# Optimization experiments

Measured on AMD Instinct MI355X. Metric: run time of the kernel, lower is better.

The kernel has to match this reference:

```python
import jax, jax.numpy as jnp
import numpy as np
from math import pi as PI

K = 32
CUTOFF = 10.0
F = 128          # num_filters (also num_gaussians)
H = 256          # in_channels
N_CLASSES = 7
N_IND = 8
LOG2 = float(np.log(2.0))


def _ssp(x):
    # ShiftedSoftplus
    return jax.nn.softplus(x) - LOG2


def _gaussian_smearing(d):
    # d: [E, 1] -> [E, F]; torch_geometric GaussianSmearing(start=0, stop=cutoff)
    offset = jnp.linspace(0.0, CUTOFF, F, dtype=d.dtype)            # [F]
    coeff = -0.5 / (offset[1] - offset[0]) ** 2
    return jnp.exp(coeff * (d - offset[None, :]) ** 2)


def setup_inputs() -> dict:
    key = jax.random.key(0)
    ks = jax.random.split(key, 24)
    Nq, Nc, B = 8192, 16384, 8
    box = 20.0
    pos_query = jax.random.uniform(ks[0], (Nq, 3), dtype=jnp.float32) * box
    pos_ctx = jax.random.uniform(ks[1], (Nc, 3), dtype=jnp.float32) * box
    node_attr_ctx = jax.random.normal(ks[2], (Nc, H), dtype=jnp.float32)
    batch_query = jnp.sort(jax.random.randint(ks[3], (Nq,), 0, B)).astype(jnp.int32)
    batch_ctx = jnp.sort(jax.random.randint(ks[4], (Nc,), 0, B)).astype(jnp.int32)

    def lin_w(k, fin, fout):
        return (jax.random.normal(k, (fin, fout), dtype=jnp.float32) / np.sqrt(fin)).astype(jnp.float32)

    return {
        "pos_query": pos_query,
        "pos_ctx": pos_ctx,
        "node_attr_ctx": node_attr_ctx,
        "batch_query": batch_query,
        "batch_ctx": batch_ctx,
        "lin1_w": lin_w(ks[5], H, F),                 # bias=False
        "lin2_w": lin_w(ks[6], F, F),
        "lin2_b": jnp.zeros((F,), jnp.float32),
        "nn1_w": lin_w(ks[7], F, F),
        "nn1_b": jnp.zeros((F,), jnp.float32),
        "nn2_w": lin_w(ks[8], F, F),
        "nn2_b": jnp.zeros((F,), jnp.float32),
        "cls1_w": lin_w(ks[9], F, F),
        "cls1_b": jnp.zeros((F,), jnp.float32),
        "cls2_w": lin_w(ks[10], F, N_CLASSES),
        "cls2_b": jnp.zeros((N_CLASSES,), jnp.float32),
        "prop1_w": lin_w(ks[11], F, F),
        "prop1_b": jnp.zeros((F,), jnp.float32),
        "prop2_w": lin_w(ks[12], F, N_IND),
        "prop2_b": jnp.zeros((N_IND,), jnp.float32),
    }


def reference(pos_query, pos_ctx, node_attr_ctx, batch_query, batch_ctx,
              lin1_w, lin2_w, lin2_b, nn1_w, nn1_b, nn2_w, nn2_b,
              cls1_w, cls1_b, cls2_w, cls2_b, prop1_w, prop1_b, prop2_w, prop2_b):
    Nq = pos_query.shape[0]

    # --- batch-aware kNN: for each query, k nearest context points in same graph ---
    d2 = (jnp.sum(pos_query ** 2, -1)[:, None]
          + jnp.sum(pos_ctx ** 2, -1)[None, :]
          - 2.0 * (pos_query @ pos_ctx.T))                            # [Nq, Nc]
    same = batch_query[:, None] == batch_ctx[None, :]
    d2 = jnp.where(same, d2, jnp.inf)
    _, nbr = jax.lax.top_k(-d2, K)                                    # [Nq, K] ctx indices

    # --- gather neighbor data; each query owns exactly K contiguous edges ---
    diff = pos_query[:, None, :] - pos_ctx[nbr]                       # [Nq, K, 3]
    dist = jnp.sqrt(jnp.sum(diff ** 2, -1)).reshape(-1, 1)            # [E, 1]
    attr_j = node_attr_ctx[nbr].reshape(Nq * K, -1)                   # [E, H]

    # --- per-edge filter network on distance expansion ---
    W = _ssp(_gaussian_smearing(dist) @ nn1_w + nn1_b) @ nn2_w + nn2_b  # [E, F]

    h = (W * (attr_j @ lin1_w)) @ lin2_w + lin2_b                     # [E, F]

    # --- cosine cutoff envelope ---
    C = 0.5 * (jnp.cos(dist * (PI / CUTOFF)) + 1.0)
    C = C * (dist <= CUTOFF) * (dist >= 0.0)
    h = h * C                                                         # [E, F]

    # scatter_add by query index == sum over the K contiguous edges per query
    y = jnp.sum(h.reshape(Nq, K, F), axis=1)                          # [Nq, F]

    y_cls = _ssp(y @ cls1_w + cls1_b) @ cls2_w + cls2_b               # [Nq, 7]
    y_ind = _ssp(y @ prop1_w + prop1_b) @ prop2_w + prop2_b           # [Nq, 8]
    return (y_cls, y_ind)
```

## Files before the change

### kernel.cpp

```cpp
#include <hip/hip_runtime.h>
#include <math.h>

#define K 32
#define F 128
#define H 256
#define TAB 4096
#define QB 8
#define BMAX 16
#define RCUT2 100.0f
#define KBINS 64
#define BINCAP 2560
#define BCAP 128
#define FP 132
#define FRR 16

__device__ __forceinline__ float ssp(float x) {
    return fmaxf(x, 0.0f) + log1pf(expf(-fabsf(x))) - 0.69314718055994531f;
}

__device__ __forceinline__ float d2f4(float4 p, float qx, float qy, float qz) {
    float dx = qx - p.x;
    float dy = qy - p.y;
    float dz = qz - p.z;
    return fmaf(dz, dz, fmaf(dy, dy, dx * dx));
}

__global__ __launch_bounds__(256) void prep_kernel(const int* __restrict__ bc, int Nc,
                                                   int* __restrict__ ctx_start,
                                                   const float* __restrict__ posc,
                                                   float4* __restrict__ posc4) {
    int blk = blockIdx.x;
    int tid = threadIdx.x;
    if (blk == 0) {
        if (tid <= BMAX) {
            int b = tid;
            int lo = 0, hi = Nc;
            while (lo < hi) {
                int mid = (lo + hi) >> 1;
                if (bc[mid] < b) lo = mid + 1; else hi = mid;
            }
            ctx_start[b] = lo;
        }
    } else {
        int i = (blk - 1) * 256 + tid;
        if (i < Nc)
            posc4[i] = make_float4(posc[i * 3 + 0], posc[i * 3 + 1], posc[i * 3 + 2], 0.0f);
    }
}


__device__ __forceinline__ void feat_body(char* smem, const float* __restrict__ attr,
                                          const float* __restrict__ lin1_w,
                                          float* __restrict__ ctx_feat, int Nc,
                                          int blk, int tid) {
    float (*sa)[H] = (float (*)[H])smem;
    int r0 = blk * FRR;
    int f = tid & 63;
    int g = tid >> 6;

    {
        float4* dst = (float4*)sa;
        const int total = FRR * H / 4;
        if (r0 + FRR <= Nc) {
            const float4* src = (const float4*)(attr + (size_t)r0 * H);
            for (int i = tid; i < total; i += 256) dst[i] = src[i];
        } else {
            for (int i = tid; i < total; i += 256) {
                int r = i / (H / 4);
                if (r0 + r < Nc) dst[i] = ((const float4*)(attr + (size_t)r0 * H))[i];
                else dst[i] = make_float4(0.0f, 0.0f, 0.0f, 0.0f);
            }
        }
    }
    __syncthreads();

    float acc0[4], acc1[4];
#pragma unroll
    for (int r = 0; r < 4; ++r) { acc0[r] = 0.0f; acc1[r] = 0.0f; }
    for (int k = 0; k < H; k += 4) {
        float wa0 = lin1_w[(k + 0) * F + f];
        float wa1 = lin1_w[(k + 1) * F + f];
        float wa2 = lin1_w[(k + 2) * F + f];
        float wa3 = lin1_w[(k + 3) * F + f];
        float wb0 = lin1_w[(k + 0) * F + f + 64];
        float wb1 = lin1_w[(k + 1) * F + f + 64];
        float wb2 = lin1_w[(k + 2) * F + f + 64];
        float wb3 = lin1_w[(k + 3) * F + f + 64];
#pragma unroll
        for (int r = 0; r < 4; ++r) {
            float4 a4 = *(const float4*)&sa[g * 4 + r][k];
            acc0[r] = fmaf(a4.x, wa0, acc0[r]);
            acc0[r] = fmaf(a4.y, wa1, acc0[r]);
            acc0[r] = fmaf(a4.z, wa2, acc0[r]);
            acc0[r] = fmaf(a4.w, wa3, acc0[r]);
            acc1[r] = fmaf(a4.x, wb0, acc1[r]);
            acc1[r] = fmaf(a4.y, wb1, acc1[r]);
            acc1[r] = fmaf(a4.z, wb2, acc1[r]);
            acc1[r] = fmaf(a4.w, wb3, acc1[r]);
        }
    }
#pragma unroll
    for (int r = 0; r < 4; ++r) {
        int row = r0 + g * 4 + r;
        if (row < Nc) {
            ctx_feat[(size_t)row * F + f] = acc0[r];
            ctx_feat[(size_t)row * F + f + 64] = acc1[r];
        }
    }
}

__device__ __forceinline__ void knn_body(char* smem, const float* __restrict__ posq,
                                         const float4* __restrict__ posc4,
                                         const int* __restrict__ bq,
                                         const int* __restrict__ ctx_start,
                                         int* __restrict__ nbr, int Nq,
                                         int blk, int tid) {
    unsigned char (*sbin)[BINCAP] = (unsigned char (*)[BINCAP])(smem);
    int (*hist)[KBINS]            = (int (*)[KBINS])(smem + 10240);
    unsigned (*bkey)[BCAP]        = (unsigned (*)[BCAP])(smem + 11264);
    int (*bidx)[BCAP]             = (int (*)[BCAP])(smem + 13312);
    int* s_nwin                   = (int*)(smem + 15360);
    int* s_nbnd                   = (int*)(smem + 15376);

    int lane = tid & 63;
    int w = tid >> 6;
    int q = blk * 4 + w;
    bool active = q < Nq;
    int qc = active ? q : 0;

    hist[w][lane] = 0;
    if (lane == 0) { s_nwin[w] = 0; s_nbnd[w] = 0; }

    float qx = posq[qc * 3 + 0];
    float qy = posq[qc * 3 + 1];
    float qz = posq[qc * 3 + 2];
    int b = bq[qc];
    int c0 = ctx_start[b];
    int c1 = ctx_start[b + 1];
    int seg = active ? (c1 - c0) : 0;
    __syncthreads();

    const float SCALE = (float)KBINS / RCUT2;
    int farc = -1;

    for (int i = lane; i < seg; i += 64) {
        float d2 = d2f4(posc4[c0 + i], qx, qy, qz);
        int bin = 255;
        if (d2 < RCUT2) {
            bin = (int)(d2 * SCALE);
            atomicAdd(&hist[w][bin], 1);
        }
        if (i < BINCAP) sbin[w][i] = (unsigned char)bin;
    }
    __syncthreads();

    int h = hist[w][lane];
    int inc = h;
#pragma unroll
    for (int off = 1; off < 64; off <<= 1) {
        int v = __shfl_up(inc, off);
        if (lane >= off) inc += v;
    }
    unsigned long long bal = __ballot(inc >= K);
    int T, below;
    if (bal) {
        T = __ffsll(bal) - 1;
        below = __shfl(inc, T) - __shfl(h, T);
    } else {
        T = KBINS;
        below = __shfl(inc, 63);
    }

    for (int i = lane; i < seg; i += 64) {
        int c = c0 + i;
        int bin;
        if (i < BINCAP) bin = sbin[w][i];
        else {
            float d2 = d2f4(posc4[c], qx, qy, qz);
            bin = (d2 < RCUT2) ? (int)(d2 * SCALE) : 255;
        }
        if (bin < T) {
            int p = atomicAdd(&s_nwin[w], 1);
            nbr[(size_t)q * K + p] = c;
        } else if (bin == T) {
            int p = atomicAdd(&s_nbnd[w], 1);
            if (p < BCAP) {
                float d2 = d2f4(posc4[c], qx, qy, qz);
                bkey[w][p] = __float_as_uint(d2);
                bidx[w][p] = c;
            }
        } else if (bin == 255) {
            farc = c;
        }
    }
#pragma unroll
    for (int off = 1; off < 64; off <<= 1) farc = max(farc, __shfl_xor(farc, off));
    if (farc < 0) farc = c0;
    __syncthreads();

    if (!active) return;
    int nb = min(s_nbnd[w], BCAP);
    int m = K - s_nwin[w];
    for (int it = 0; it < m; ++it) {
        unsigned long long bestkey = 0xFFFFFFFFFFFFFFFFull;
        int bestp = -1;
        for (int p = lane; p < nb; p += 64) {
            unsigned kk = bkey[w][p];
            if (kk != 0xFFFFFFFFu) {
                unsigned long long pk = ((unsigned long long)kk << 32) | (unsigned)bidx[w][p];
                if (pk < bestkey) { bestkey = pk; bestp = p; }
            }
        }
#pragma unroll
        for (int off = 1; off < 64; off <<= 1) {
            unsigned long long ok = __shfl_xor(bestkey, off);
            int op = __shfl_xor(bestp, off);
            if (ok < bestkey) { bestkey = ok; bestp = op; }
        }
        if (lane == 0) {
            if (bestp >= 0 && bestkey != 0xFFFFFFFFFFFFFFFFull) {
                nbr[(size_t)q * K + below + it] = (int)(bestkey & 0xFFFFFFFFu);
                bkey[w][bestp] = 0xFFFFFFFFu;
            } else {
                nbr[(size_t)q * K + below + it] = farc;
            }
        }
        __asm__ volatile("" ::: "memory");
    }
}

__device__ __forceinline__ void wtab_body(char* smem, const float* __restrict__ nn1_w,
                                          const float* __restrict__ nn1_b,
                                          const float* __restrict__ nn2_w,
                                          const float* __restrict__ nn2_b,
                                          float2* __restrict__ wt2,
                                          int blk, int tid) {
    float (*sg)[F] = (float (*)[F])smem;
    float (*st)[F] = (float (*)[F])(smem + 8704);
    int t0 = blk * FRR;
    int f = tid & (F - 1);
    int g = tid >> 7;

    const float delta = 10.0f / 127.0f;
    const float coeff = -0.5f / (delta * delta);
    float off = (float)f * delta;
    for (int r = g; r < 17; r += 2) {
        float dist = (float)(t0 + r) * (10.0f / (float)TAB);
        float d = dist - off;
        sg[r][f] = expf(coeff * d * d);
    }
    __syncthreads();

    float acc[9];
#pragma unroll
    for (int r = 0; r < 9; ++r) acc[r] = 0.0f;
    for (int j = 0; j < F; j += 4) {
        float w0 = nn1_w[(j + 0) * F + f];
        float w1 = nn1_w[(j + 1) * F + f];
        float w2 = nn1_w[(j + 2) * F + f];
        float w3 = nn1_w[(j + 3) * F + f];
#pragma unroll
        for (int r = 0; r < 9; ++r) {
            float4 a4 = *(const float4*)&sg[g * 8 + r][j];
            acc[r] = fmaf(a4.x, w0, acc[r]);
            acc[r] = fmaf(a4.y, w1, acc[r]);
            acc[r] = fmaf(a4.z, w2, acc[r]);
            acc[r] = fmaf(a4.w, w3, acc[r]);
        }
    }
    float b1 = nn1_b[f];
#pragma unroll
    for (int r = 0; r < 9; ++r) st[g * 8 + r][f] = ssp(acc[r] + b1);
    __syncthreads();

#pragma unroll
    for (int r = 0; r < 9; ++r) acc[r] = 0.0f;
    for (int j = 0; j < F; j += 4) {
        float w0 = nn2_w[(j + 0) * F + f];
        float w1 = nn2_w[(j + 1) * F + f];
        float w2 = nn2_w[(j + 2) * F + f];
        float w3 = nn2_w[(j + 3) * F + f];
#pragma unroll
        for (int r = 0; r < 9; ++r) {
            float4 a4 = *(const float4*)&st[g * 8 + r][j];
            acc[r] = fmaf(a4.x, w0, acc[r]);
            acc[r] = fmaf(a4.y, w1, acc[r]);
            acc[r] = fmaf(a4.z, w2, acc[r]);
            acc[r] = fmaf(a4.w, w3, acc[r]);
        }
    }
    float b2 = nn2_b[f];
#pragma unroll
    for (int i = 0; i < 8; ++i) {
        int t = t0 + g * 8 + i;
        wt2[(size_t)t * F + f] = make_float2(acc[i] + b2, acc[i + 1] + b2);
    }
}

__global__ __launch_bounds__(256) void phase2_kernel(const float* __restrict__ attr,
                                                     const float* __restrict__ lin1_w,
                                                     float* __restrict__ ctx_feat, int Nc,
                                                     const float* __restrict__ posq,
                                                     const float4* __restrict__ posc4,
                                                     const int* __restrict__ bq,
                                                     const int* __restrict__ ctx_start,
                                                     int* __restrict__ nbr, int Nq,
                                                     const float* __restrict__ nn1_w,
                                                     const float* __restrict__ nn1_b,
                                                     const float* __restrict__ nn2_w,
                                                     const float* __restrict__ nn2_b,
                                                     float2* __restrict__ wt2,
                                                     int knnB, int wtabB) {
    __shared__ __align__(16) char smem[17408];
    int blk = blockIdx.x;
    int tid = threadIdx.x;
    if (blk < knnB) {
        knn_body(smem, posq, posc4, bq, ctx_start, nbr, Nq, blk, tid);
    } else if (blk < knnB + wtabB) {
        wtab_body(smem, nn1_w, nn1_b, nn2_w, nn2_b, wt2, blk - knnB, tid);
    } else {
        feat_body(smem, attr, lin1_w, ctx_feat, Nc, blk - knnB - wtabB, tid);
    }
}

__global__ __launch_bounds__(256) void agghead_kernel(const float* __restrict__ posq,
                                                      const float4* __restrict__ posc4,
                                                      const int* __restrict__ nbr,
                                                      const float* __restrict__ ctx_feat,
                                                      const float2* __restrict__ wt2,
                                                      const float* __restrict__ lin2_w,
                                                      const float* __restrict__ lin2_b,
                                                      const float* __restrict__ cls1_w,
                                                      const float* __restrict__ cls1_b,
                                                      const float* __restrict__ cls2_w,
                                                      const float* __restrict__ cls2_b,
                                                      const float* __restrict__ prop1_w,
                                                      const float* __restrict__ prop1_b,
                                                      const float* __restrict__ prop2_w,
                                                      const float* __restrict__ prop2_b,
                                                      float* __restrict__ out_cls,
                                                      float* __restrict__ out_ind, int Nq) {
    const int QH = QB / 2;
    int q0 = blockIdx.x * QB;
    int tid = threadIdx.x;

    __shared__ int   sj[QB * K];
    __shared__ float sC[QB * K];
    __shared__ int   si0[QB * K];
    __shared__ float sfr[QB * K];
    __shared__ float sa[QB][F];
    __shared__ float ssc[QB];
    __shared__ float sy[QB][FP];
    __shared__ float sc1[QB][FP];
    __shared__ float sp1[QB][FP];

    {
        int qq = tid >> 5;
        int q = q0 + qq;
        if (q >= Nq) q = Nq - 1;
        int j = nbr[(size_t)q * K + (tid & 31)];
        float4 p = posc4[j];
        float dx = posq[q * 3 + 0] - p.x;
        float dy = posq[q * 3 + 1] - p.y;
        float dz = posq[q * 3 + 2] - p.z;
        float dist = sqrtf(fmaf(dz, dz, fmaf(dy, dy, dx * dx)));
        float C = 0.0f, fr = 0.0f;
        int i0 = 0;
        if (dist <= 10.0f) {
            C = 0.5f * (cosf(dist * 0.31415926535897931f) + 1.0f);
            float u = dist * ((float)TAB / 10.0f);
            i0 = (int)u;
            if (i0 > TAB - 1) i0 = TAB - 1;
            fr = u - (float)i0;
        }
        sj[tid] = j; sC[tid] = C; si0[tid] = i0; sfr[tid] = fr;
        float cs = C;
#pragma unroll
        for (int off = 1; off < 32; off <<= 1) cs += __shfl_xor(cs, off);
        if ((tid & 31) == 0) ssc[qq] = cs;
    }
    __syncthreads();

    int f = tid & (F - 1);
    int g = tid >> 7;

    {
        float acc[QH] = {0.0f, 0.0f, 0.0f, 0.0f};
#pragma unroll 2
        for (int k = 0; k < K; ++k) {
#pragma unroll
            for (int i = 0; i < QH; ++i) {
                int e = (g * QH + i) * K + k;
                int j = sj[e];
                float C = sC[e];
                int i0 = si0[e];
                float fr = sfr[e];
                float2 w = wt2[(size_t)i0 * F + f];
                float a = ctx_feat[(size_t)j * F + f];
                float W = fmaf(fr, w.y - w.x, w.x);
                acc[i] = fmaf(C * W, a, acc[i]);
            }
        }
#pragma unroll
        for (int i = 0; i < QH; ++i) sa[g * QH + i][f] = acc[i];
    }
    __syncthreads();

    {
        float y[QH];
        float lb = lin2_b[f];
#pragma unroll
        for (int i = 0; i < QH; ++i) y[i] = ssc[g * QH + i] * lb;
        for (int j = 0; j < F; j += 4) {
            float w0 = lin2_w[(j + 0) * F + f];
            float w1 = lin2_w[(j + 1) * F + f];
            float w2 = lin2_w[(j + 2) * F + f];
            float w3 = lin2_w[(j + 3) * F + f];
#pragma unroll
            for (int i = 0; i < QH; ++i) {
                float4 a4 = *(const float4*)&sa[g * QH + i][j];
                y[i] = fmaf(a4.x, w0, y[i]);
                y[i] = fmaf(a4.y, w1, y[i]);
                y[i] = fmaf(a4.z, w2, y[i]);
                y[i] = fmaf(a4.w, w3, y[i]);
            }
        }
#pragma unroll
        for (int i = 0; i < QH; ++i) sy[g * QH + i][f] = y[i];
    }
    __syncthreads();

    {
        float c1[QH], p1[QH];
        float cb = cls1_b[f], pb = prop1_b[f];
#pragma unroll
        for (int i = 0; i < QH; ++i) { c1[i] = cb; p1[i] = pb; }
        for (int j = 0; j < F; j += 4) {
            float wc0 = cls1_w[(j + 0) * F + f];
            float wc1 = cls1_w[(j + 1) * F + f];
            float wc2 = cls1_w[(j + 2) * F + f];
            float wc3 = cls1_w[(j + 3) * F + f];
            float wp0 = prop1_w[(j + 0) * F + f];
            float wp1 = prop1_w[(j + 1) * F + f];
            float wp2 = prop1_w[(j + 2) * F + f];
            float wp3 = prop1_w[(j + 3) * F + f];
#pragma unroll
            for (int i = 0; i < QH; ++i) {
                float4 y4 = *(const float4*)&sy[g * QH + i][j];
                c1[i] = fmaf(y4.x, wc0, c1[i]);
                c1[i] = fmaf(y4.y, wc1, c1[i]);
                c1[i] = fmaf(y4.z, wc2, c1[i]);
                c1[i] = fmaf(y4.w, wc3, c1[i]);
                p1[i] = fmaf(y4.x, wp0, p1[i]);
                p1[i] = fmaf(y4.y, wp1, p1[i]);
                p1[i] = fmaf(y4.z, wp2, p1[i]);
                p1[i] = fmaf(y4.w, wp3, p1[i]);
            }
        }
#pragma unroll
        for (int i = 0; i < QH; ++i) {
            sc1[g * QH + i][f] = ssp(c1[i]);
            sp1[g * QH + i][f] = ssp(p1[i]);
        }
    }
    __syncthreads();

    {
        int qq = tid >> 5;
        int c = tid & 31;
        int q = q0 + qq;
        if (q < Nq && c < 15) {
            if (c < 7) {
                float acc = cls2_b[c];
                for (int j = 0; j < F; ++j) acc = fmaf(sc1[qq][j], cls2_w[j * 7 + c], acc);
                out_cls[(size_t)q * 7 + c] = acc;
            } else {
                int cc = c - 7;
                float acc = prop2_b[cc];
                for (int j = 0; j < F; ++j) acc = fmaf(sp1[qq][j], prop2_w[j * 8 + cc], acc);
                out_ind[(size_t)q * 8 + cc] = acc;
            }
        }
    }
}

extern "C" void kernel_launch(void* const* d_in, const int* in_sizes, int n_in,
                              void* d_out, int out_size, void* d_ws, size_t ws_size,
                              hipStream_t stream) {
    const float* posq   = (const float*)d_in[0];
    const float* posc   = (const float*)d_in[1];
    const float* attr   = (const float*)d_in[2];
    const int*   bq     = (const int*)d_in[3];
    const int*   bc     = (const int*)d_in[4];
    const float* lin1_w = (const float*)d_in[5];
    const float* lin2_w = (const float*)d_in[6];
    const float* lin2_b = (const float*)d_in[7];
    const float* nn1_w  = (const float*)d_in[8];
    const float* nn1_b  = (const float*)d_in[9];
    const float* nn2_w  = (const float*)d_in[10];
    const float* nn2_b  = (const float*)d_in[11];
    const float* cls1_w = (const float*)d_in[12];
    const float* cls1_b = (const float*)d_in[13];
    const float* cls2_w = (const float*)d_in[14];
    const float* cls2_b = (const float*)d_in[15];
    const float* prop1_w = (const float*)d_in[16];
    const float* prop1_b = (const float*)d_in[17];
    const float* prop2_w = (const float*)d_in[18];
    const float* prop2_b = (const float*)d_in[19];
    (void)n_in; (void)out_size; (void)ws_size;

    int Nq = in_sizes[0] / 3;
    int Nc = in_sizes[1] / 3;

    char* ws = (char*)d_ws;
    size_t off = 0;
    auto alloc = [&](size_t bytes) {
        off = (off + 255) & ~(size_t)255;
        void* p = ws + off;
        off += bytes;
        return p;
    };
    int*    ctx_start = (int*)alloc((BMAX + 1) * sizeof(int));
    int*    nbr       = (int*)alloc((size_t)Nq * K * sizeof(int));
    float*  ctx_feat  = (float*)alloc((size_t)Nc * F * sizeof(float));
    float2* wt2       = (float2*)alloc((size_t)TAB * F * sizeof(float2));
    float4* posc4     = (float4*)alloc((size_t)Nc * sizeof(float4));

    float* out_cls = (float*)d_out;
    float* out_ind = out_cls + (size_t)Nq * 7;

    int padB  = (Nc + 255) / 256;
    int featB = (Nc + FRR - 1) / FRR;
    int knnB  = (Nq + 3) / 4;
    int wtabB = TAB / FRR;

    prep_kernel<<<dim3(1 + padB), dim3(256), 0, stream>>>(bc, Nc, ctx_start, posc, posc4);
    phase2_kernel<<<dim3(knnB + wtabB + featB), dim3(256), 0, stream>>>(
        attr, lin1_w, ctx_feat, Nc,
        posq, posc4, bq, ctx_start, nbr, Nq,
        nn1_w, nn1_b, nn2_w, nn2_b, wt2, knnB, wtabB);
    agghead_kernel<<<dim3((Nq + QB - 1) / QB), dim3(256), 0, stream>>>(
        posq, posc4, nbr, ctx_feat, wt2,
        lin2_w, lin2_b, cls1_w, cls1_b, cls2_w, cls2_b,
        prop1_w, prop1_b, prop2_w, prop2_b, out_cls, out_ind, Nq);
}
```

Measured before the change: 133.7 us.

## Split fused phase2 kernel into separate knn, feat, wtab kernels; pack edge data

The combined phase2 kernel, which dispatched knn, weight-table and feature blocks by block index, is split into three separate kernel launches, each with its own tailored shared memory. The agghead kernel now packs the per-edge C, fraction, table index and neighbor index into one float4 in shared memory instead of four separate arrays, so each edge is read with a single vector LDS load. The split lets each kernel use only the registers and LDS it needs, which can raise occupancy. The cost is that the three independent workloads now run one after another on the stream instead of concurrently, plus two extra launches.

New measurement: 134.4 us. About the same (+0.5%).

```diff
diff --git a/kernel.cpp b/kernel.cpp
--- a/kernel.cpp
+++ b/kernel.cpp
@@ -48,12 +48,12 @@
     }
 }
 
-
-__device__ __forceinline__ void feat_body(char* smem, const float* __restrict__ attr,
-                                          const float* __restrict__ lin1_w,
-                                          float* __restrict__ ctx_feat, int Nc,
-                                          int blk, int tid) {
-    float (*sa)[H] = (float (*)[H])smem;
+__global__ __launch_bounds__(256) void feat_kernel(const float* __restrict__ attr,
+                                                   const float* __restrict__ lin1_w,
+                                                   float* __restrict__ ctx_feat, int Nc) {
+    __shared__ float sa[FRR][H];
+    int blk = blockIdx.x;
+    int tid = threadIdx.x;
     int r0 = blk * FRR;
     int f = tid & 63;
     int g = tid >> 6;
@@ -109,22 +109,21 @@
     }
 }
 
-__device__ __forceinline__ void knn_body(char* smem, const float* __restrict__ posq,
-                                         const float4* __restrict__ posc4,
-                                         const int* __restrict__ bq,
-                                         const int* __restrict__ ctx_start,
-                                         int* __restrict__ nbr, int Nq,
-                                         int blk, int tid) {
-    unsigned char (*sbin)[BINCAP] = (unsigned char (*)[BINCAP])(smem);
-    int (*hist)[KBINS]            = (int (*)[KBINS])(smem + 10240);
-    unsigned (*bkey)[BCAP]        = (unsigned (*)[BCAP])(smem + 11264);
-    int (*bidx)[BCAP]             = (int (*)[BCAP])(smem + 13312);
-    int* s_nwin                   = (int*)(smem + 15360);
-    int* s_nbnd                   = (int*)(smem + 15376);
-
+__global__ __launch_bounds__(256) void knn_kernel(const float* __restrict__ posq,
+                                                  const float4* __restrict__ posc4,
+                                                  const int* __restrict__ bq,
+                                                  const int* __restrict__ ctx_start,
+                                                  int* __restrict__ nbr, int Nq) {
+    __shared__ unsigned char sbin[4][BINCAP];
+    __shared__ int hist[4][KBINS];
+    __shared__ unsigned bkey[4][BCAP];
+    __shared__ int bidx[4][BCAP];
+    __shared__ int s_nwin[4], s_nbnd[4];
+
+    int tid = threadIdx.x;
     int lane = tid & 63;
     int w = tid >> 6;
-    int q = blk * 4 + w;
+    int q = blockIdx.x * 4 + w;
     bool active = q < Nq;
     int qc = active ? q : 0;
 
@@ -229,15 +228,15 @@
     }
 }
 
-__device__ __forceinline__ void wtab_body(char* smem, const float* __restrict__ nn1_w,
-                                          const float* __restrict__ nn1_b,
-                                          const float* __restrict__ nn2_w,
-                                          const float* __restrict__ nn2_b,
-                                          float2* __restrict__ wt2,
-                                          int blk, int tid) {
-    float (*sg)[F] = (float (*)[F])smem;
-    float (*st)[F] = (float (*)[F])(smem + 8704);
-    int t0 = blk * FRR;
+__global__ __launch_bounds__(256) void wtab_kernel(const float* __restrict__ nn1_w,
+                                                   const float* __restrict__ nn1_b,
+                                                   const float* __restrict__ nn2_w,
+                                                   const float* __restrict__ nn2_b,
+                                                   float2* __restrict__ wt2) {
+    __shared__ float sg[17][F];
+    __shared__ float st[17][F];
+    int t0 = blockIdx.x * FRR;
+    int tid = threadIdx.x;
     int f = tid & (F - 1);
     int g = tid >> 7;
 
@@ -294,32 +293,6 @@
     for (int i = 0; i < 8; ++i) {
         int t = t0 + g * 8 + i;
         wt2[(size_t)t * F + f] = make_float2(acc[i] + b2, acc[i + 1] + b2);
-    }
-}
-
-__global__ __launch_bounds__(256) void phase2_kernel(const float* __restrict__ attr,
-                                                     const float* __restrict__ lin1_w,
-                                                     float* __restrict__ ctx_feat, int Nc,
-                                                     const float* __restrict__ posq,
-                                                     const float4* __restrict__ posc4,
-                                                     const int* __restrict__ bq,
-                                                     const int* __restrict__ ctx_start,
-                                                     int* __restrict__ nbr, int Nq,
-                                                     const float* __restrict__ nn1_w,
-                                                     const float* __restrict__ nn1_b,
-                                                     const float* __restrict__ nn2_w,
-                                                     const float* __restrict__ nn2_b,
-                                                     float2* __restrict__ wt2,
-                                                     int knnB, int wtabB) {
-    __shared__ __align__(16) char smem[17408];
-    int blk = blockIdx.x;
-    int tid = threadIdx.x;
-    if (blk < knnB) {
-        knn_body(smem, posq, posc4, bq, ctx_start, nbr, Nq, blk, tid);
-    } else if (blk < knnB + wtabB) {
-        wtab_body(smem, nn1_w, nn1_b, nn2_w, nn2_b, wt2, blk - knnB, tid);
-    } else {
-        feat_body(smem, attr, lin1_w, ctx_feat, Nc, blk - knnB - wtabB, tid);
     }
 }
 
@@ -344,10 +317,7 @@
     int q0 = blockIdx.x * QB;
     int tid = threadIdx.x;
 
-    __shared__ int   sj[QB * K];
-    __shared__ float sC[QB * K];
-    __shared__ int   si0[QB * K];
-    __shared__ float sfr[QB * K];
+    __shared__ float4 sedge[QB * K];
     __shared__ float sa[QB][F];
     __shared__ float ssc[QB];
     __shared__ float sy[QB][FP];
@@ -373,7 +343,7 @@
             if (i0 > TAB - 1) i0 = TAB - 1;
             fr = u - (float)i0;
         }
-        sj[tid] = j; sC[tid] = C; si0[tid] = i0; sfr[tid] = fr;
+        sedge[tid] = make_float4(C, fr, __int_as_float(i0), __int_as_float(j));
         float cs = C;
 #pragma unroll
         for (int off = 1; off < 32; off <<= 1) cs += __shfl_xor(cs, off);
@@ -390,11 +360,11 @@
         for (int k = 0; k < K; ++k) {
 #pragma unroll
             for (int i = 0; i < QH; ++i) {
-                int e = (g * QH + i) * K + k;
-                int j = sj[e];
-                float C = sC[e];
-                int i0 = si0[e];
-                float fr = sfr[e];
+                float4 e4 = sedge[(g * QH + i) * K + k];
+                float C = e4.x;
+                float fr = e4.y;
+                int i0 = __float_as_int(e4.z);
+                int j = __float_as_int(e4.w);
                 float2 w = wt2[(size_t)i0 * F + f];
                 float a = ctx_feat[(size_t)j * F + f];
                 float W = fmaf(fr, w.y - w.x, w.x);
@@ -535,10 +505,9 @@
     int wtabB = TAB / FRR;
 
     prep_kernel<<<dim3(1 + padB), dim3(256), 0, stream>>>(bc, Nc, ctx_start, posc, posc4);
-    phase2_kernel<<<dim3(knnB + wtabB + featB), dim3(256), 0, stream>>>(
-        attr, lin1_w, ctx_feat, Nc,
-        posq, posc4, bq, ctx_start, nbr, Nq,
-        nn1_w, nn1_b, nn2_w, nn2_b, wt2, knnB, wtabB);
+    knn_kernel<<<dim3(knnB), dim3(256), 0, stream>>>(posq, posc4, bq, ctx_start, nbr, Nq);
+    feat_kernel<<<dim3(featB), dim3(256), 0, stream>>>(attr, lin1_w, ctx_feat, Nc);
+    wtab_kernel<<<dim3(wtabB), dim3(256), 0, stream>>>(nn1_w, nn1_b, nn2_w, nn2_b, wt2);
     agghead_kernel<<<dim3((Nq + QB - 1) / QB), dim3(256), 0, stream>>>(
         posq, posc4, nbr, ctx_feat, wt2,
         lin2_w, lin2_b, cls1_w, cls1_b, cls2_w, cls2_b,
```
